# Optimization experiments

Hardware: AMD Instinct MI355X
Metric: run time of the kernel (lower is better)

Reference implementation:

```python
import jax, jax.numpy as jnp
import numpy as np

S = 8192
D = 512

def setup_inputs() -> dict:
    key = jax.random.key(0)
    k1, k2, k3, k4 = jax.random.split(key, 4)
    token_encodings = jax.random.normal(k1, (S, D), dtype=jnp.float32)
    # causal mask: True where attention is disallowed (strictly upper triangular)
    mask = jnp.triu(jnp.ones((S, S), dtype=bool), k=1)
    W_q = jax.random.normal(k2, (D, D), dtype=jnp.float32) * (1.0 / np.sqrt(D))
    W_k = jax.random.normal(k3, (D, D), dtype=jnp.float32) * (1.0 / np.sqrt(D))
    W_v = jax.random.normal(k4, (D, D), dtype=jnp.float32) * (1.0 / np.sqrt(D))
    return {"token_encodings": token_encodings, "mask": mask, "W_q": W_q, "W_k": W_k, "W_v": W_v}

def reference(token_encodings, mask, W_q, W_k, W_v):
    # nn.Linear(bias=False): y = x @ W^T
    q = token_encodings @ W_q.T  # [S, D]
    k = token_encodings @ W_k.T  # [S, D]
    v = token_encodings @ W_v.T  # [S, D]
    scale = jnp.asarray(k.shape[1], dtype=q.dtype) ** 0.5
    sims = (q @ k.T) / scale  # [S, S]
    sims = jnp.where(mask, jnp.asarray(-1e9, dtype=sims.dtype), sims)
    attn = jax.nn.softmax(sims, axis=1)
    return attn @ v  # [S, D]
```

## Files before the change

### kernel.cpp

```cpp
#include <hip/hip_runtime.h>
#include <stdint.h>

typedef _Float16 f16;
typedef _Float16 f16x8 __attribute__((ext_vector_type(8)));
typedef _Float16 f16x4 __attribute__((ext_vector_type(4)));
typedef float f32x4 __attribute__((ext_vector_type(4)));

#define S_TOK 8192
#define DDIM  512
#define L2E   1.44269504088896340736f
#define QSCALE 0.04419417382415922f
#define NSLOT 320
#define GTOT  8320

__device__ __forceinline__ void gload_lds16(const void* g, void* l) {
  __builtin_amdgcn_global_load_lds((const __attribute__((address_space(1))) void*)g,
                                   (__attribute__((address_space(3))) void*)l, 16, 0, 0);
}

template <int C>
__device__ __forceinline__ float fdpp(float x) {
  return __builtin_bit_cast(float,
      __builtin_amdgcn_update_dpp(0, __builtin_bit_cast(int, x), C, 0xF, 0xF, true));
}
__device__ __forceinline__ float rowmax16(float x) {
  x = fmaxf(x, fdpp<0xB1>(x));
  x = fmaxf(x, fdpp<0x4E>(x));
  x = fmaxf(x, fdpp<0x141>(x));
  x = fmaxf(x, fdpp<0x140>(x));
  return x;
}
__device__ __forceinline__ float rowsum16(float x) {
  x += fdpp<0xB1>(x);
  x += fdpp<0x4E>(x);
  x += fdpp<0x141>(x);
  x += fdpp<0x140>(x);
  return x;
}

__global__ __launch_bounds__(256) void k_convert(
    const float* __restrict__ X, const float* __restrict__ Wq,
    const float* __restrict__ Wk, const float* __restrict__ Wv,
    f16* __restrict__ Xh, f16* __restrict__ Wh, int* __restrict__ tp) {
  const int SD = S_TOK * DDIM;
  const int DD = DDIM * DDIM;
  int gi = blockIdx.x * 256 + threadIdx.x;
  if (gi < NSLOT) tp[gi] = -1;
  int i4 = gi * 4;
  if (i4 < SD) {
    f32x4 v = *(const f32x4*)(X + i4);
    f16x4 h = {(f16)v[0], (f16)v[1], (f16)v[2], (f16)v[3]};
    *(f16x4*)(Xh + i4) = h;
  } else {
    int j = i4 - SD;
    int mat = j >> 18;
    const float* src = (mat == 0) ? Wq : (mat == 1 ? Wk : Wv);
    f32x4 v = *(const f32x4*)(src + (j & (DD - 1)));
    f16x4 h = {(f16)v[0], (f16)v[1], (f16)v[2], (f16)v[3]};
    *(f16x4*)(Wh + j) = h;
  }
}

__global__ __launch_bounds__(256) void k_proj(
    const f16* __restrict__ Xh, const f16* __restrict__ Wh,
    f16* __restrict__ Qh, f16* __restrict__ KB, f16* __restrict__ VB) {
  __shared__ __align__(16) char Al[128 * 128];
  __shared__ __align__(16) char Bl[128 * 128];
  const int tid = threadIdx.x;
  const int w = tid >> 6, lane = tid & 63;
  const int m0 = blockIdx.x * 128;
  const int n0 = blockIdx.y * 128;
  const int wr = (w >> 1) * 64;
  const int wc = (w & 1) * 64;

  f32x4 acc[4][4];
#pragma unroll
  for (int i = 0; i < 4; ++i)
#pragma unroll
    for (int j = 0; j < 4; ++j) acc[i][j] = (f32x4){0.f, 0.f, 0.f, 0.f};

  const char* Xb = (const char*)Xh;
  const char* Wb = (const char*)Wh;

  for (int kb = 0; kb < DDIM; kb += 64) {
    __syncthreads();
#pragma unroll
    for (int i = 0; i < 4; ++i) {
      int ch = w * 4 + i;
      int srow = lane >> 3;
      int scol = ((lane & 7) * 16) ^ (srow << 4);
      gload_lds16(Xb + (size_t)(m0 + ch * 8 + srow) * 1024 + kb * 2 + scol, Al + ch * 1024);
      gload_lds16(Wb + (size_t)(n0 + ch * 8 + srow) * 1024 + kb * 2 + scol, Bl + ch * 1024);
    }
    __syncthreads();
#pragma unroll
    for (int ks = 0; ks < 2; ++ks) {
      f16x8 a[4], b[4];
#pragma unroll
      for (int mf = 0; mf < 4; ++mf) {
        int row = wr + mf * 16 + (lane & 15);
        int col = (ks * 64 + ((lane >> 4) * 16)) ^ ((row & 7) << 4);
        a[mf] = *(const f16x8*)(Al + row * 128 + col);
      }
#pragma unroll
      for (int nf = 0; nf < 4; ++nf) {
        int row = wc + nf * 16 + (lane & 15);
        int col = (ks * 64 + ((lane >> 4) * 16)) ^ ((row & 7) << 4);
        b[nf] = *(const f16x8*)(Bl + row * 128 + col);
      }
#pragma unroll
      for (int mf = 0; mf < 4; ++mf)
#pragma unroll
        for (int nf = 0; nf < 4; ++nf)
          acc[mf][nf] = __builtin_amdgcn_mfma_f32_16x16x32_f16(a[mf], b[nf], acc[mf][nf], 0, 0, 0);
    }
  }
  int mat = n0 >> 9;
  int nbase = n0 & 511;
  if (mat == 2) {
#pragma unroll
    for (int mf = 0; mf < 4; ++mf) {
      int R0 = m0 + wr + mf * 16 + (lane >> 4) * 4;
      int K = R0 >> 5;
      int lhi = ((R0 >> 3) & 3) * 16;
      int j0 = R0 & 7;
#pragma unroll
      for (int nf = 0; nf < 4; ++nf) {
        int col = nbase + wc + nf * 16 + (lane & 15);
        f16x4 h = {(f16)acc[mf][nf][0], (f16)acc[mf][nf][1],
                   (f16)acc[mf][nf][2], (f16)acc[mf][nf][3]};
        *(f16x4*)((char*)VB + (size_t)(K * 32 + (col >> 4)) * 1024 +
                  (lhi + (col & 15)) * 16 + j0 * 2) = h;
      }
    }
  } else if (mat == 1) {
#pragma unroll
    for (int mf = 0; mf < 4; ++mf)
#pragma unroll
      for (int nf = 0; nf < 4; ++nf)
#pragma unroll
        for (int r = 0; r < 4; ++r) {
          int token = m0 + wr + mf * 16 + (lane >> 4) * 4 + r;
          int d = nbase + wc + nf * 16 + (lane & 15);
          size_t byte = (size_t)(token >> 5) * 32768 + (size_t)((token >> 4) & 1) * 16384
                      + (size_t)(d >> 5) * 1024
                      + (token & 15) * 16 + ((d >> 3) & 3) * 256 + (d & 7) * 2;
          *(f16*)((char*)KB + byte) = (f16)acc[mf][nf][r];
        }
  } else {
    float scale = QSCALE;
#pragma unroll
    for (int mf = 0; mf < 4; ++mf)
#pragma unroll
      for (int nf = 0; nf < 4; ++nf)
#pragma unroll
        for (int r = 0; r < 4; ++r) {
          int row = m0 + wr + mf * 16 + (lane >> 4) * 4 + r;
          int col = nbase + wc + nf * 16 + (lane & 15);
          Qh[(size_t)row * DDIM + col] = (f16)(acc[mf][nf][r] * scale);
        }
  }
}

__global__ __launch_bounds__(512, 2) void k_flash(
    const f16* __restrict__ Qh, const f16* __restrict__ KBg,
    const f16* __restrict__ VBg, f16* __restrict__ Opart,
    float* __restrict__ Mpart, float* __restrict__ Lpart,
    int* __restrict__ TilePart) {
  __shared__ __align__(16) char Kl[2][32768];
  __shared__ __align__(16) char Vl[2][32768];
  __shared__ __align__(16) char Pl[8][2][1152];

  const int tid = threadIdx.x;
  const int w = tid >> 6, lane = tid & 63;
  const int l15 = lane & 15, l4 = lane >> 4;

  int bid = blockIdx.x;
  int b = (bid & 7) * 32 + (bid >> 3);
  int g  = (GTOT * b) >> 8;
  int g1 = (GTOT * (b + 1)) >> 8;
  int t = 0;
  while (2 * (t + 1) * (t + 2) <= g) ++t;

  const char* Kb = (const char*)KBg;
  const char* Vb = (const char*)VBg;

#define STAGEK(KB_, BI) do {                                                   \
    const char* ks_ = Kb + (size_t)((KB_) >> 5) * 32768;                       \
    _Pragma("unroll")                                                          \
    for (int i_ = 0; i_ < 4; ++i_) {                                           \
      int ch_ = w * 4 + i_;                                                    \
      gload_lds16(ks_ + ch_ * 1024 + lane * 16, Kl[BI] + ch_ * 1024);          \
    } } while (0)

#define STAGEV(KB_, BI) do {                                                   \
    const char* vs_ = Vb + (size_t)(KB_) * 1024;                               \
    _Pragma("unroll")                                                          \
    for (int i_ = 0; i_ < 4; ++i_) {                                           \
      int ch_ = w * 4 + i_;                                                    \
      gload_lds16(vs_ + ch_ * 1024 + lane * 16, Vl[BI] + ch_ * 1024);          \
    } } while (0)

#define SOFTMAX(KB_, Pdst) do {                                                \
    float p0[4], p1[4], mx[4];                                                 \
    int qrb = q0 + w * 16 + l4 * 4;                                            \
    int kc = (KB_) + l15;                                                      \
    _Pragma("unroll")                                                          \
    for (int r = 0; r < 4; ++r) {                                              \
      int qr = qrb + r;                                                        \
      float x0 = (kc      <= qr) ? s0[r] : -3.0e38f;                           \
      float x1 = (kc + 16 <= qr) ? s1[r] : -3.0e38f;                           \
      p0[r] = x0; p1[r] = x1;                                                  \
      mx[r] = rowmax16(fmaxf(x0, x1));                                         \
    }                                                                          \
    bool need = (mx[0] > mreg[0] + 8.f) || (mx[1] > mreg[1] + 8.f) ||          \
                (mx[2] > mreg[2] + 8.f) || (mx[3] > mreg[3] + 8.f);            \
    if (__any(need)) {                                                         \
      float alpha[4];                                                          \
      _Pragma("unroll")                                                        \
      for (int r = 0; r < 4; ++r) {                                            \
        float mn = fmaxf(mreg[r], mx[r]);                                      \
        alpha[r] = exp2f((mreg[r] - mn) * L2E);                                \
        lreg[r] *= alpha[r];                                                   \
        mreg[r] = mn;                                                          \
      }                                                                        \
      _Pragma("unroll")                                                        \
      for (int nf = 0; nf < 32; ++nf) {                                        \
        acc[nf][0] *= alpha[0];                                                \
        acc[nf][1] *= alpha[1];                                                \
        acc[nf][2] *= alpha[2];                                                \
        acc[nf][3] *= alpha[3];                                                \
      }                                                                        \
    }                                                                          \
    _Pragma("unroll")                                                          \
    for (int r = 0; r < 4; ++r) {                                              \
      int qr = qrb + r;                                                        \
      p0[r] = (kc      <= qr) ? exp2f((p0[r] - mreg[r]) * L2E) : 0.f;          \
      p1[r] = (kc + 16 <= qr) ? exp2f((p1[r] - mreg[r]) * L2E) : 0.f;          \
    }                                                                          \
    _Pragma("unroll")                                                          \
    for (int r = 0; r < 4; ++r) {                                              \
      int row = l4 * 4 + r;                                                    \
      *(f16*)((Pdst) + row * 72 + l15 * 2)      = (f16)p0[r];                  \
      *(f16*)((Pdst) + row * 72 + 32 + l15 * 2) = (f16)p1[r];                  \
    }                                                                          \
    _Pragma("unroll")                                                          \
    for (int r = 0; r < 4; ++r)                                                \
      lreg[r] += rowsum16(p0[r] + p1[r]);                                      \
  } while (0)

#define QKT(BUF) do {                                                          \
    s0 = (f32x4){0.f, 0.f, 0.f, 0.f};                                          \
    s1 = (f32x4){0.f, 0.f, 0.f, 0.f};                                          \
    const char* kp_ = (BUF) + lane * 16;                                       \
    __builtin_amdgcn_s_setprio(1);                                             \
    _Pragma("unroll")                                                          \
    for (int ks = 0; ks < 16; ++ks) {                                          \
      f16x8 kf0 = *(const f16x8*)(kp_ + ks * 1024);                            \
      s0 = __builtin_amdgcn_mfma_f32_16x16x32_f16(qf[ks], kf0, s0, 0, 0, 0);   \
      f16x8 kf1 = *(const f16x8*)(kp_ + 16384 + ks * 1024);                    \
      s1 = __builtin_amdgcn_mfma_f32_16x16x32_f16(qf[ks], kf1, s1, 0, 0, 0);   \
    }                                                                          \
    __builtin_amdgcn_s_setprio(0); } while (0)

#define PV(BI) do {                                                            \
    const char* vp_ = Vl[BI] + lane * 16;                                      \
    const char* Pp_ = Pw + (BI) * 1152;                                        \
    f16x8 pa_ = *(const f16x8*)(Pp_ + l15 * 72 + l4 * 16);                     \
    __builtin_amdgcn_s_setprio(1);                                             \
    _Pragma("unroll")                                                          \
    for (int nf = 0; nf < 32; ++nf) {                                          \
      f16x8 vb_ = *(const f16x8*)(vp_ + nf * 1024);                            \
      acc[nf] = __builtin_amdgcn_mfma_f32_16x16x32_f16(pa_, vb_, acc[nf], 0, 0, 0); \
    }                                                                          \
    __builtin_amdgcn_s_setprio(0); } while (0)

#define FUSED(KBUF, VBI) do {                                                  \
    s0 = (f32x4){0.f, 0.f, 0.f, 0.f};                                          \
    s1 = (f32x4){0.f, 0.f, 0.f, 0.f};                                          \
    const char* kp_ = (KBUF) + lane * 16;                                      \
    const char* vp_ = Vl[VBI] + lane * 16;                                     \
    const char* Pp_ = Pw + (VBI) * 1152;                                       \
    f16x8 pa_ = *(const f16x8*)(Pp_ + l15 * 72 + l4 * 16);                     \
    __builtin_amdgcn_s_setprio(1);                                             \
    _Pragma("unroll")                                                          \
    for (int ks = 0; ks < 16; ++ks) {                                          \
      f16x8 kf0 = *(const f16x8*)(kp_ + ks * 1024);                            \
      s0 = __builtin_amdgcn_mfma_f32_16x16x32_f16(qf[ks], kf0, s0, 0, 0, 0);   \
      f16x8 vb0 = *(const f16x8*)(vp_ + (2 * ks) * 1024);                      \
      acc[2 * ks] = __builtin_amdgcn_mfma_f32_16x16x32_f16(pa_, vb0, acc[2 * ks], 0, 0, 0); \
      f16x8 kf1 = *(const f16x8*)(kp_ + 16384 + ks * 1024);                    \
      s1 = __builtin_amdgcn_mfma_f32_16x16x32_f16(qf[ks], kf1, s1, 0, 0, 0);   \
      f16x8 vb1 = *(const f16x8*)(vp_ + (2 * ks + 1) * 1024);                  \
      acc[2 * ks + 1] = __builtin_amdgcn_mfma_f32_16x16x32_f16(pa_, vb1, acc[2 * ks + 1], 0, 0, 0); \
    }                                                                          \
    __builtin_amdgcn_s_setprio(0); } while (0)

  char* Pw = (char*)Pl + (size_t)w * 2304;

  while (g < g1) {
    int Ct  = 2 * t * (t + 1);
    int Ct1 = 2 * (t + 1) * (t + 2);
    int gend = min(g1, Ct1);
    int n = gend - g;
    int kb0 = (g - Ct) * 32;
    int q0 = t * 128;
    int slot = b + t;

    f16x8 qf[16];
    {
      const f16* qp = Qh + (size_t)(q0 + w * 16 + l15) * DDIM + l4 * 8;
#pragma unroll
      for (int ks = 0; ks < 16; ++ks) qf[ks] = *(const f16x8*)(qp + ks * 32);
    }
    f32x4 acc[32];
#pragma unroll
    for (int i = 0; i < 32; ++i) acc[i] = (f32x4){0.f, 0.f, 0.f, 0.f};
    float mreg[4], lreg[4];
#pragma unroll
    for (int r = 0; r < 4; ++r) { mreg[r] = -3.0e38f; lreg[r] = 0.f; }
    f32x4 s0, s1;

    STAGEK(kb0, 0);
    STAGEV(kb0, 0);
    asm volatile("s_waitcnt vmcnt(0)" ::: "memory");
    __builtin_amdgcn_s_barrier();
    if (n > 1) STAGEK(kb0 + 32, 1);
    QKT(Kl[0]);
    SOFTMAX(kb0, Pw);
    asm volatile("s_waitcnt lgkmcnt(0)" ::: "memory");
    if (n > 1) STAGEV(kb0 + 32, 1);

    for (int it = 1; it < n; ++it) {
      asm volatile("s_waitcnt vmcnt(4)" ::: "memory");
      __builtin_amdgcn_s_barrier();
      if (it + 1 < n) STAGEK(kb0 + (it + 1) * 32, (it + 1) & 1);
      FUSED(Kl[it & 1], (it - 1) & 1);
      __builtin_amdgcn_s_barrier();
      if (it + 1 < n) STAGEV(kb0 + (it + 1) * 32, (it + 1) & 1);
      SOFTMAX(kb0 + it * 32, Pw + (it & 1) * 1152);
      asm volatile("s_waitcnt lgkmcnt(0)" ::: "memory");
    }

    asm volatile("s_waitcnt vmcnt(0)" ::: "memory");
    __builtin_amdgcn_s_barrier();
    PV((n - 1) & 1);
    __builtin_amdgcn_s_barrier();

    {
      float inv[4];
#pragma unroll
      for (int r = 0; r < 4; ++r) inv[r] = (lreg[r] > 0.f) ? 1.f / lreg[r] : 0.f;
      f16* op = Opart + (size_t)slot * (128 * 512);
      int rowb = w * 16 + l4 * 4;
#pragma unroll
      for (int nf = 0; nf < 32; ++nf) {
        int col = nf * 16 + l15;
#pragma unroll
        for (int r = 0; r < 4; ++r)
          op[(size_t)(rowb + r) * 512 + col] = (f16)(acc[nf][r] * inv[r]);
      }
      if (l15 == 0) {
#pragma unroll
        for (int r = 0; r < 4; ++r) {
          Mpart[slot * 128 + rowb + r] = mreg[r];
          Lpart[slot * 128 + rowb + r] = lreg[r];
        }
      }
      if (tid == 0) TilePart[slot] = t;
    }
    g = gend;
    ++t;
  }
#undef STAGEK
#undef STAGEV
#undef SOFTMAX
#undef QKT
#undef PV
#undef FUSED
}

__global__ __launch_bounds__(256) void k_reduce(
    const f16* __restrict__ Opart, const float* __restrict__ Mpart,
    const float* __restrict__ Lpart, const int* __restrict__ TilePart,
    float* __restrict__ out) {
  __shared__ int tp[NSLOT];
  __shared__ int sl[16];
  __shared__ int scnt;
  int tid = threadIdx.x;
  int t = blockIdx.x >> 2, rg = blockIdx.x & 3;
  for (int s = tid; s < NSLOT; s += 256) tp[s] = TilePart[s];
  __syncthreads();
  if (tid == 0) {
    int c = 0;
    for (int s = 0; s < NSLOT; ++s)
      if (tp[s] == t && c < 16) sl[c++] = s;
    scnt = c;
  }
  __syncthreads();
  int cnt = scnt;
  int rowIn = rg * 32 + (tid >> 3);
  int row = t * 128 + rowIn;
  int col0 = (tid & 7) * 64;

  float M = -3.0e38f;
  for (int i = 0; i < cnt; ++i) M = fmaxf(M, Mpart[sl[i] * 128 + rowIn]);
  float a[64];
#pragma unroll
  for (int j = 0; j < 64; ++j) a[j] = 0.f;
  float denom = 0.f;
  for (int i = 0; i < cnt; ++i) {
    int s = sl[i];
    float m = Mpart[s * 128 + rowIn];
    float l = Lpart[s * 128 + rowIn];
    float wgt = exp2f((m - M) * L2E) * l;
    denom += wgt;
    const f16* op = Opart + (size_t)s * 65536 + rowIn * 512 + col0;
#pragma unroll
    for (int v = 0; v < 8; ++v) {
      f16x8 x = *(const f16x8*)(op + v * 8);
#pragma unroll
      for (int j = 0; j < 8; ++j) a[v * 8 + j] += wgt * (float)x[j];
    }
  }
  float inv = (denom > 0.f) ? 1.f / denom : 0.f;
  float* o = out + (size_t)row * 512 + col0;
#pragma unroll
  for (int j = 0; j < 64; ++j) o[j] = a[j] * inv;
}

extern "C" void kernel_launch(void* const* d_in, const int* in_sizes, int n_in,
                              void* d_out, int out_size, void* d_ws, size_t ws_size,
                              hipStream_t stream) {
  const float* X  = (const float*)d_in[0];
  const float* Wq = (const float*)d_in[2];
  const float* Wk = (const float*)d_in[3];
  const float* Wv = (const float*)d_in[4];
  float* out = (float*)d_out;

  char* ws = (char*)d_ws;
  f16*   Opart = (f16*)(ws);
  float* Mpart = (float*)(ws + (40u << 20));
  float* Lpart = (float*)(ws + (41u << 20));
  int*   TileP = (int*)(ws + (42u << 20));
  f16* Qh = (f16*)(ws + (43u << 20));
  f16* KB = (f16*)(ws + (51u << 20));
  f16* VB = (f16*)(ws + (59u << 20));
  f16* Xh = (f16*)(ws + (67u << 20));
  f16* Wh = (f16*)(ws + (75u << 20));

  k_convert<<<4864, 256, 0, stream>>>(X, Wq, Wk, Wv, Xh, Wh, TileP);
  dim3 gp(64, 12);
  k_proj<<<gp, 256, 0, stream>>>(Xh, Wh, Qh, KB, VB);
  k_flash<<<256, 512, 0, stream>>>(Qh, KB, VB, Opart, Mpart, Lpart, TileP);
  k_reduce<<<256, 256, 0, stream>>>(Opart, Mpart, Lpart, TileP, out);
}
```

Measured before the change: 212.3 us.

## Store flash partial outputs in MFMA fragment layout and restructure reduce

The flash kernel now writes each thread's accumulator fragment as one contiguous f16x4 vector store, in a fragment-native layout, instead of strided scalar f16 stores. The reduce kernel is rewritten to read that layout with one 512-thread block per 128-row tile and per-thread 4-row weights. The goal is fully coalesced wide stores and loads of the partials. In exchange the reduce launches only 64 blocks, which lowers parallelism, and its final fp32 output stores are strided at 16-column granularity.

```diff
diff --git a/kernel.cpp b/kernel.cpp
--- a/kernel.cpp
+++ b/kernel.cpp
@@ -351,15 +351,14 @@
       float inv[4];
 #pragma unroll
       for (int r = 0; r < 4; ++r) inv[r] = (lreg[r] > 0.f) ? 1.f / lreg[r] : 0.f;
-      f16* op = Opart + (size_t)slot * (128 * 512);
+      char* op = (char*)Opart + (size_t)slot * 131072;
+#pragma unroll
+      for (int nf = 0; nf < 32; ++nf) {
+        f16x4 h = {(f16)(acc[nf][0] * inv[0]), (f16)(acc[nf][1] * inv[1]),
+                   (f16)(acc[nf][2] * inv[2]), (f16)(acc[nf][3] * inv[3])};
+        *(f16x4*)(op + nf * 4096 + tid * 8) = h;
+      }
       int rowb = w * 16 + l4 * 4;
-#pragma unroll
-      for (int nf = 0; nf < 32; ++nf) {
-        int col = nf * 16 + l15;
-#pragma unroll
-        for (int r = 0; r < 4; ++r)
-          op[(size_t)(rowb + r) * 512 + col] = (f16)(acc[nf][r] * inv[r]);
-      }
       if (l15 == 0) {
 #pragma unroll
         for (int r = 0; r < 4; ++r) {
@@ -380,7 +379,7 @@
 #undef FUSED
 }
 
-__global__ __launch_bounds__(256) void k_reduce(
+__global__ __launch_bounds__(512) void k_reduce(
     const f16* __restrict__ Opart, const float* __restrict__ Mpart,
     const float* __restrict__ Lpart, const int* __restrict__ TilePart,
     float* __restrict__ out) {
@@ -388,8 +387,8 @@
   __shared__ int sl[16];
   __shared__ int scnt;
   int tid = threadIdx.x;
-  int t = blockIdx.x >> 2, rg = blockIdx.x & 3;
-  for (int s = tid; s < NSLOT; s += 256) tp[s] = TilePart[s];
+  int t = blockIdx.x;
+  for (int s = tid; s < NSLOT; s += 512) tp[s] = TilePart[s];
   __syncthreads();
   if (tid == 0) {
     int c = 0;
@@ -399,34 +398,51 @@
   }
   __syncthreads();
   int cnt = scnt;
-  int rowIn = rg * 32 + (tid >> 3);
-  int row = t * 128 + rowIn;
-  int col0 = (tid & 7) * 64;
-
-  float M = -3.0e38f;
-  for (int i = 0; i < cnt; ++i) M = fmaxf(M, Mpart[sl[i] * 128 + rowIn]);
-  float a[64];
-#pragma unroll
-  for (int j = 0; j < 64; ++j) a[j] = 0.f;
-  float denom = 0.f;
+  const int w = tid >> 6, lane = tid & 63;
+  const int l15 = lane & 15, l4 = lane >> 4;
+  const int rowb = w * 16 + l4 * 4;
+
+  float M[4];
+#pragma unroll
+  for (int r = 0; r < 4; ++r) M[r] = -3.0e38f;
   for (int i = 0; i < cnt; ++i) {
     int s = sl[i];
-    float m = Mpart[s * 128 + rowIn];
-    float l = Lpart[s * 128 + rowIn];
-    float wgt = exp2f((m - M) * L2E) * l;
-    denom += wgt;
-    const f16* op = Opart + (size_t)s * 65536 + rowIn * 512 + col0;
-#pragma unroll
-    for (int v = 0; v < 8; ++v) {
-      f16x8 x = *(const f16x8*)(op + v * 8);
-#pragma unroll
-      for (int j = 0; j < 8; ++j) a[v * 8 + j] += wgt * (float)x[j];
-    }
-  }
-  float inv = (denom > 0.f) ? 1.f / denom : 0.f;
-  float* o = out + (size_t)row * 512 + col0;
-#pragma unroll
-  for (int j = 0; j < 64; ++j) o[j] = a[j] * inv;
+#pragma unroll
+    for (int r = 0; r < 4; ++r) M[r] = fmaxf(M[r], Mpart[s * 128 + rowb + r]);
+  }
+
+  f32x4 a[32];
+#pragma unroll
+  for (int nf = 0; nf < 32; ++nf) a[nf] = (f32x4){0.f, 0.f, 0.f, 0.f};
+  float denom[4] = {0.f, 0.f, 0.f, 0.f};
+
+  for (int i = 0; i < cnt; ++i) {
+    int s = sl[i];
+    float wgt[4];
+#pragma unroll
+    for (int r = 0; r < 4; ++r) {
+      float m = Mpart[s * 128 + rowb + r];
+      float l = Lpart[s * 128 + rowb + r];
+      wgt[r] = exp2f((m - M[r]) * L2E) * l;
+      denom[r] += wgt[r];
+    }
+    const char* op = (const char*)Opart + (size_t)s * 131072 + tid * 8;
+#pragma unroll
+    for (int nf = 0; nf < 32; ++nf) {
+      f16x4 x = *(const f16x4*)(op + nf * 4096);
+#pragma unroll
+      for (int r = 0; r < 4; ++r) a[nf][r] += wgt[r] * (float)x[r];
+    }
+  }
+  float inv[4];
+#pragma unroll
+  for (int r = 0; r < 4; ++r) inv[r] = (denom[r] > 0.f) ? 1.f / denom[r] : 0.f;
+  float* ob = out + (size_t)(t * 128 + rowb) * 512 + l15;
+#pragma unroll
+  for (int nf = 0; nf < 32; ++nf)
+#pragma unroll
+    for (int r = 0; r < 4; ++r)
+      ob[(size_t)r * 512 + nf * 16] = a[nf][r] * inv[r];
 }
 
 extern "C" void kernel_launch(void* const* d_in, const int* in_sizes, int n_in,
@@ -453,5 +469,5 @@
   dim3 gp(64, 12);
   k_proj<<<gp, 256, 0, stream>>>(Xh, Wh, Qh, KB, VB);
   k_flash<<<256, 512, 0, stream>>>(Qh, KB, VB, Opart, Mpart, Lpart, TileP);
-  k_reduce<<<256, 256, 0, stream>>>(Opart, Mpart, Lpart, TileP, out);
-}
+  k_reduce<<<64, 512, 0, stream>>>(Opart, Mpart, Lpart, TileP, out);
+}
```

Measured after the change: 263.8 us. 24.2% more time.
